# Kernel tuning notes

Measured on AMD Instinct MI355X. Metric: run time of the kernel, lower is better.

The kernel has to match this reference:

```python
import jax, jax.numpy as jnp
import numpy as np

N = 500_000      # total nodes across all graphs in batch
B = 128          # batch_size (number of graphs)
S = 128          # state_size
D = 128          # aggregated_size


def setup_inputs() -> dict:
    key = jax.random.key(0)
    k1, k2, k3, k4, k5, k6 = jax.random.split(key, 6)
    nodes = jax.random.normal(k1, (N, S), dtype=jnp.float32)
    owner_masks = jax.random.randint(k2, (B, N), 0, 2, dtype=jnp.int32)
    # Linear params (torch Linear: y = x @ W.T + b); store W as [in, out] for x @ W
    scale = 1.0 / np.sqrt(S)
    Wt = jax.random.uniform(k3, (S, D), jnp.float32, -scale, scale)
    bt = jax.random.uniform(k4, (D,), jnp.float32, -scale, scale)
    Wg = jax.random.uniform(k5, (S, D), jnp.float32, -scale, scale)
    bg = jax.random.uniform(k6, (D,), jnp.float32, -scale, scale)
    return {"nodes": nodes, "owner_masks": owner_masks,
            "Wt": Wt, "bt": bt, "Wg": Wg, "bg": bg}


def reference(nodes, owner_masks, Wt, bt, Wg, bg):
    # gates = sigmoid(nodes @ Wg + bg)   [N, D]
    gates = jax.nn.sigmoid(nodes @ Wg + bg)
    # data = nodes @ Wt + bt             [N, D]
    data = nodes @ Wt + bt
    # pooled = owner_masks.float() @ (data * gates)   [B, D]
    return owner_masks.astype(jnp.float32) @ (data * gates)
```

## Files before the change

### kernel.cpp

```cpp
#include <hip/hip_runtime.h>


#define NTOT   500000
#define NBLK   500
#define NCHUNK 15625

typedef unsigned long long u64;
typedef unsigned int u32;

typedef __attribute__((ext_vector_type(8))) unsigned short ushort8;
typedef __bf16 bf16x8 __attribute__((ext_vector_type(8)));
typedef __attribute__((ext_vector_type(4))) float f32x4;

static __device__ __forceinline__ unsigned short f2bf(float f) {
  u32 u = __float_as_uint(f);
  u += 0x7fffu + ((u >> 16) & 1u);
  return (unsigned short)(u >> 16);
}

static __device__ __forceinline__ u64 pack4(unsigned short a, unsigned short b,
                                            unsigned short c, unsigned short d) {
  return (u64)a | ((u64)b << 16) | ((u64)c << 32) | ((u64)d << 48);
}

static __device__ __forceinline__ u32 bits2bf2(u32 byte, int j) {
  return ((byte >> j) & 1u ? 0x3F80u : 0u) | ((byte >> (j + 1)) & 1u ? 0x3F800000u : 0u);
}

template <bool ATOMIC>
__global__ __launch_bounds__(256, 2)
void agg_main(const float* __restrict__ nodes, const int* __restrict__ masks,
              const float* __restrict__ Wt, const float* __restrict__ bt,
              const float* __restrict__ Wg, const float* __restrict__ bg,
              float* __restrict__ outp) {
  __shared__ __align__(16) unsigned short nodes_s[32][136];
  __shared__ __align__(16) u64 bits[128][17];
  __shared__ __align__(16) unsigned short vt_s[128][40];

  const int tid = threadIdx.x;
  const int lane = tid & 63;
  const int w = tid >> 6;
  const int q = lane >> 4;
  const int r = lane & 15;

  const int bid = blockIdx.x;
  const int c0 = (int)(((long long)bid * NCHUNK) / NBLK);
  const int c1 = (int)(((long long)(bid + 1) * NCHUNK) / NBLK);
  const int nch = c1 - c0;
  const int n0 = c0 * 32;

  bf16x8 Wf[2][4][2];
  float btr[2], bgr[2];
#pragma unroll
  for (int nt = 0; nt < 2; ++nt) {
    const int d = w * 32 + nt * 16 + r;
    btr[nt] = bt[d];
    bgr[nt] = bg[d];
#pragma unroll
    for (int ks = 0; ks < 4; ++ks) {
      ushort8 ft, fg;
#pragma unroll
      for (int j = 0; j < 8; ++j) {
        const int k = ks * 32 + q * 8 + j;
        ft[j] = f2bf(Wt[k * 128 + d]);
        fg[j] = f2bf(Wg[k * 128 + d]);
      }
      Wf[0][ks][nt] = __builtin_bit_cast(bf16x8, ft);
      Wf[1][ks][nt] = __builtin_bit_cast(bf16x8, fg);
    }
  }

  {
    const int row0 = w * 32;
    int cur[32], nxt[32];
#pragma unroll
    for (int k = 0; k < 32; ++k)
      cur[k] = masks[(size_t)(row0 + k) * NTOT + n0 + lane];
#pragma unroll
    for (int g = 0; g < 16; ++g) {
      if (g < 15) {
#pragma unroll
        for (int k = 0; k < 32; ++k)
          nxt[k] = masks[(size_t)(row0 + k) * NTOT + n0 + (g + 1) * 64 + lane];
      }
      u64 v = 0;
#pragma unroll
      for (int k = 0; k < 32; ++k) {
        u64 bl = __ballot(cur[k] != 0);
        if (lane == k) v = bl;
      }
      if (lane < 32) bits[row0 + lane][g] = v;
      if (g < 15) {
#pragma unroll
        for (int k = 0; k < 32; ++k) cur[k] = nxt[k];
      }
    }
  }

  f32x4 acc[8][2];
  const f32x4 fzero = {0.f, 0.f, 0.f, 0.f};
#pragma unroll
  for (int i = 0; i < 8; ++i) {
    acc[i][0] = fzero;
    acc[i][1] = fzero;
  }

  float4 nf[4];
  auto issue = [&](int cloc) {
    const int k0 = n0 + cloc * 32;
#pragma unroll
    for (int it = 0; it < 4; ++it) {
      const int flat = it * 256 + tid;
      const int nrow = flat >> 5, nc4 = flat & 31;
      nf[it] = *(const float4*)(nodes + (size_t)(k0 + nrow) * 128 + nc4 * 4);
    }
  };

  issue(0);
  __syncthreads();

  const u32* bitw = (const u32*)bits;

  for (int c = 0; c < nch; ++c) {
    if (c) __syncthreads();
#pragma unroll
    for (int it = 0; it < 4; ++it) {
      const int flat = it * 256 + tid;
      const int nrow = flat >> 5, nc4 = flat & 31;
      *(u64*)&nodes_s[nrow][nc4 * 4] =
          pack4(f2bf(nf[it].x), f2bf(nf[it].y), f2bf(nf[it].z), f2bf(nf[it].w));
    }
    __syncthreads();
    if (c + 1 < nch) issue(c + 1);

    f32x4 aD[2][2], aG[2][2];
#pragma unroll
    for (int i = 0; i < 2; ++i)
#pragma unroll
      for (int j = 0; j < 2; ++j) { aD[i][j] = fzero; aG[i][j] = fzero; }
#pragma unroll
    for (int ks = 0; ks < 4; ++ks) {
      bf16x8 a0 = *(const bf16x8*)&nodes_s[r][ks * 32 + q * 8];
      bf16x8 a1 = *(const bf16x8*)&nodes_s[16 + r][ks * 32 + q * 8];
#pragma unroll
      for (int nt = 0; nt < 2; ++nt) {
        aD[0][nt] = __builtin_amdgcn_mfma_f32_16x16x32_bf16(a0, Wf[0][ks][nt], aD[0][nt], 0, 0, 0);
        aD[1][nt] = __builtin_amdgcn_mfma_f32_16x16x32_bf16(a1, Wf[0][ks][nt], aD[1][nt], 0, 0, 0);
        aG[0][nt] = __builtin_amdgcn_mfma_f32_16x16x32_bf16(a0, Wf[1][ks][nt], aG[0][nt], 0, 0, 0);
        aG[1][nt] = __builtin_amdgcn_mfma_f32_16x16x32_bf16(a1, Wf[1][ks][nt], aG[1][nt], 0, 0, 0);
      }
    }

#pragma unroll
    for (int mt = 0; mt < 2; ++mt)
#pragma unroll
      for (int nt = 0; nt < 2; ++nt) {
        const int d = w * 32 + nt * 16 + r;
        unsigned short t[4];
#pragma unroll
        for (int reg = 0; reg < 4; ++reg) {
          const float x = aD[mt][nt][reg] + btr[nt];
          const float g = aG[mt][nt][reg] + bgr[nt];
          t[reg] = f2bf(x / (1.f + __expf(-g)));
        }
        *(u64*)&vt_s[d][mt * 16 + q * 4] = pack4(t[0], t[1], t[2], t[3]);
      }

    bf16x8 bfr[2];
#pragma unroll
    for (int nt = 0; nt < 2; ++nt)
      bfr[nt] = *(const bf16x8*)&vt_s[w * 32 + nt * 16 + r][q * 8];
#pragma unroll
    for (int mt = 0; mt < 8; ++mt) {
      const u32 dw = bitw[(mt * 16 + r) * 34 + c];
      const u32 byte = (dw >> (q * 8)) & 0xffu;
      u32 p0 = bits2bf2(byte, 0), p1 = bits2bf2(byte, 2);
      u32 p2 = bits2bf2(byte, 4), p3 = bits2bf2(byte, 6);
      u32 af[4] = {p0, p1, p2, p3};
      bf16x8 a = __builtin_bit_cast(bf16x8, *(ushort8*)af);
#pragma unroll
      for (int nt = 0; nt < 2; ++nt)
        acc[mt][nt] = __builtin_amdgcn_mfma_f32_16x16x32_bf16(a, bfr[nt], acc[mt][nt], 0, 0, 0);
    }
  }

#pragma unroll
  for (int mt = 0; mt < 8; ++mt)
#pragma unroll
    for (int nt = 0; nt < 2; ++nt)
#pragma unroll
      for (int reg = 0; reg < 4; ++reg) {
        const int b = mt * 16 + q * 4 + reg;
        const int d = w * 32 + nt * 16 + r;
        if (ATOMIC)
          atomicAdd(&outp[b * 128 + d], acc[mt][nt][reg]);
        else
          outp[(size_t)bid * 16384 + b * 128 + d] = acc[mt][nt][reg];
      }
}

__global__ __launch_bounds__(256)
void agg_reduce(const float* __restrict__ part, float* __restrict__ out) {
  const int gid = blockIdx.x * 256 + threadIdx.x;
  const int i = gid & 16383;
  const int grp = gid >> 14;
  const float* p = part + (size_t)grp * 125 * 16384 + i;
  float s = 0.f;
#pragma unroll 5
  for (int g = 0; g < 125; ++g) s += p[(size_t)g * 16384];
  atomicAdd(&out[i], s);
}

extern "C" void kernel_launch(void* const* d_in, const int* in_sizes, int n_in,
                              void* d_out, int out_size, void* d_ws, size_t ws_size,
                              hipStream_t stream) {
  const float* nodes = (const float*)d_in[0];
  const int*   masks = (const int*)d_in[1];
  const float* Wt    = (const float*)d_in[2];
  const float* bt    = (const float*)d_in[3];
  const float* Wg    = (const float*)d_in[4];
  const float* bg    = (const float*)d_in[5];
  float* out = (float*)d_out;

  hipMemsetAsync(d_out, 0, (size_t)out_size * sizeof(float), stream);

  const size_t need = (size_t)NBLK * 16384 * sizeof(float);
  if (ws_size >= need) {
    agg_main<false><<<NBLK, 256, 0, stream>>>(nodes, masks, Wt, bt, Wg, bg, (float*)d_ws);
    agg_reduce<<<256, 256, 0, stream>>>((const float*)d_ws, out);
  } else {
    agg_main<true><<<NBLK, 256, 0, stream>>>(nodes, masks, Wt, bt, Wg, bg, out);
  }
}
```

Baseline: 562.5 us.

## Use 512-thread blocks, 512 workgroups, and vectorized mask-to-bit packing

Doubles the block size to 8 waves, so each wave owns 16 output columns instead of 32 and each block stages half as many node rows per thread. Mask bitpacking switches from per-element ballots to int4 vector loads, with each lane packing 16 consecutive nodes per row. The grid becomes 512 blocks so the chunk split can use a shift, and the reduce kernel is adjusted to match. The sigmoid division is also replaced with a hardware reciprocal. These changes aim to raise occupancy and memory-level parallelism on the bandwidth-bound mask read, at the cost of more barrier participants and a changed bit layout.

```diff
diff --git a/kernel.cpp b/kernel.cpp
--- a/kernel.cpp
+++ b/kernel.cpp
@@ -2,7 +2,7 @@
 
 
 #define NTOT   500000
-#define NBLK   500
+#define NBLK   512
 #define NCHUNK 15625
 
 typedef unsigned long long u64;
@@ -12,15 +12,14 @@
 typedef __bf16 bf16x8 __attribute__((ext_vector_type(8)));
 typedef __attribute__((ext_vector_type(4))) float f32x4;
 
-static __device__ __forceinline__ unsigned short f2bf(float f) {
+static __device__ __forceinline__ u32 f2bf1(float f) {
   u32 u = __float_as_uint(f);
   u += 0x7fffu + ((u >> 16) & 1u);
-  return (unsigned short)(u >> 16);
-}
-
-static __device__ __forceinline__ u64 pack4(unsigned short a, unsigned short b,
-                                            unsigned short c, unsigned short d) {
-  return (u64)a | ((u64)b << 16) | ((u64)c << 32) | ((u64)d << 48);
+  return u >> 16;
+}
+
+static __device__ __forceinline__ u32 f2bf2(float a, float b) {
+  return f2bf1(a) | (f2bf1(b) << 16);
 }
 
 static __device__ __forceinline__ u32 bits2bf2(u32 byte, int j) {
@@ -28,7 +27,7 @@
 }
 
 template <bool ATOMIC>
-__global__ __launch_bounds__(256, 2)
+__global__ __launch_bounds__(512, 4)
 void agg_main(const float* __restrict__ nodes, const int* __restrict__ masks,
               const float* __restrict__ Wt, const float* __restrict__ bt,
               const float* __restrict__ Wg, const float* __restrict__ bg,
@@ -44,73 +43,66 @@
   const int r = lane & 15;
 
   const int bid = blockIdx.x;
-  const int c0 = (int)(((long long)bid * NCHUNK) / NBLK);
-  const int c1 = (int)(((long long)(bid + 1) * NCHUNK) / NBLK);
+  const int c0 = (int)(((long long)bid * NCHUNK) >> 9);
+  const int c1 = (int)(((long long)(bid + 1) * NCHUNK) >> 9);
   const int nch = c1 - c0;
   const int n0 = c0 * 32;
 
-  bf16x8 Wf[2][4][2];
-  float btr[2], bgr[2];
-#pragma unroll
-  for (int nt = 0; nt < 2; ++nt) {
-    const int d = w * 32 + nt * 16 + r;
-    btr[nt] = bt[d];
-    bgr[nt] = bg[d];
+  {
+    const int row0 = w * 16;
+    int cb = 16 * lane;
+    if (cb >= nch * 32) cb = 0;
+    int4 cur[4], nxt[4];
+    auto ldrow = [&](int rr, int4* dst) {
+      const int* p = masks + (size_t)(row0 + rr) * NTOT + n0 + cb;
+#pragma unroll
+      for (int i = 0; i < 4; ++i) dst[i] = *(const int4*)(p + 4 * i);
+    };
+    ldrow(0, cur);
+#pragma unroll 4
+    for (int rr = 0; rr < 16; ++rr) {
+      if (rr < 15) ldrow(rr + 1, nxt);
+      const int* m = (const int*)cur;
+      u32 b = 0;
+#pragma unroll
+      for (int e = 0; e < 16; ++e) b |= (u32)(m[e] != 0) << e;
+      ((unsigned short*)bits)[(row0 + rr) * 68 + lane] = (unsigned short)b;
+#pragma unroll
+      for (int i = 0; i < 4; ++i) cur[i] = nxt[i];
+    }
+  }
+
+  bf16x8 Wf[2][4];
+  float btr, bgr;
+  {
+    const int d = w * 16 + r;
+    btr = bt[d];
+    bgr = bg[d];
 #pragma unroll
     for (int ks = 0; ks < 4; ++ks) {
-      ushort8 ft, fg;
-#pragma unroll
-      for (int j = 0; j < 8; ++j) {
-        const int k = ks * 32 + q * 8 + j;
-        ft[j] = f2bf(Wt[k * 128 + d]);
-        fg[j] = f2bf(Wg[k * 128 + d]);
+      u32 wv[4], gv[4];
+#pragma unroll
+      for (int j = 0; j < 4; ++j) {
+        const int k = ks * 32 + q * 8 + 2 * j;
+        wv[j] = f2bf2(Wt[k * 128 + d], Wt[(k + 1) * 128 + d]);
+        gv[j] = f2bf2(Wg[k * 128 + d], Wg[(k + 1) * 128 + d]);
       }
-      Wf[0][ks][nt] = __builtin_bit_cast(bf16x8, ft);
-      Wf[1][ks][nt] = __builtin_bit_cast(bf16x8, fg);
-    }
-  }
-
-  {
-    const int row0 = w * 32;
-    int cur[32], nxt[32];
-#pragma unroll
-    for (int k = 0; k < 32; ++k)
-      cur[k] = masks[(size_t)(row0 + k) * NTOT + n0 + lane];
-#pragma unroll
-    for (int g = 0; g < 16; ++g) {
-      if (g < 15) {
-#pragma unroll
-        for (int k = 0; k < 32; ++k)
-          nxt[k] = masks[(size_t)(row0 + k) * NTOT + n0 + (g + 1) * 64 + lane];
-      }
-      u64 v = 0;
-#pragma unroll
-      for (int k = 0; k < 32; ++k) {
-        u64 bl = __ballot(cur[k] != 0);
-        if (lane == k) v = bl;
-      }
-      if (lane < 32) bits[row0 + lane][g] = v;
-      if (g < 15) {
-#pragma unroll
-        for (int k = 0; k < 32; ++k) cur[k] = nxt[k];
-      }
-    }
-  }
-
-  f32x4 acc[8][2];
+      Wf[0][ks] = __builtin_bit_cast(bf16x8, *(ushort8*)wv);
+      Wf[1][ks] = __builtin_bit_cast(bf16x8, *(ushort8*)gv);
+    }
+  }
+
   const f32x4 fzero = {0.f, 0.f, 0.f, 0.f};
-#pragma unroll
-  for (int i = 0; i < 8; ++i) {
-    acc[i][0] = fzero;
-    acc[i][1] = fzero;
-  }
-
-  float4 nf[4];
+  f32x4 acc[8];
+#pragma unroll
+  for (int i = 0; i < 8; ++i) acc[i] = fzero;
+
+  float4 nf[2];
   auto issue = [&](int cloc) {
     const int k0 = n0 + cloc * 32;
 #pragma unroll
-    for (int it = 0; it < 4; ++it) {
-      const int flat = it * 256 + tid;
+    for (int it = 0; it < 2; ++it) {
+      const int flat = it * 512 + tid;
       const int nrow = flat >> 5, nc4 = flat & 31;
       nf[it] = *(const float4*)(nodes + (size_t)(k0 + nrow) * 128 + nc4 * 4);
     }
@@ -124,79 +116,69 @@
   for (int c = 0; c < nch; ++c) {
     if (c) __syncthreads();
 #pragma unroll
-    for (int it = 0; it < 4; ++it) {
-      const int flat = it * 256 + tid;
+    for (int it = 0; it < 2; ++it) {
+      const int flat = it * 512 + tid;
       const int nrow = flat >> 5, nc4 = flat & 31;
-      *(u64*)&nodes_s[nrow][nc4 * 4] =
-          pack4(f2bf(nf[it].x), f2bf(nf[it].y), f2bf(nf[it].z), f2bf(nf[it].w));
+      const u32 lo = f2bf2(nf[it].x, nf[it].y);
+      const u32 hi = f2bf2(nf[it].z, nf[it].w);
+      *(u64*)&nodes_s[nrow][nc4 * 4] = (u64)lo | ((u64)hi << 32);
     }
     __syncthreads();
     if (c + 1 < nch) issue(c + 1);
 
-    f32x4 aD[2][2], aG[2][2];
-#pragma unroll
-    for (int i = 0; i < 2; ++i)
-#pragma unroll
-      for (int j = 0; j < 2; ++j) { aD[i][j] = fzero; aG[i][j] = fzero; }
+    f32x4 aD[2], aG[2];
+    aD[0] = fzero; aD[1] = fzero; aG[0] = fzero; aG[1] = fzero;
 #pragma unroll
     for (int ks = 0; ks < 4; ++ks) {
       bf16x8 a0 = *(const bf16x8*)&nodes_s[r][ks * 32 + q * 8];
       bf16x8 a1 = *(const bf16x8*)&nodes_s[16 + r][ks * 32 + q * 8];
-#pragma unroll
-      for (int nt = 0; nt < 2; ++nt) {
-        aD[0][nt] = __builtin_amdgcn_mfma_f32_16x16x32_bf16(a0, Wf[0][ks][nt], aD[0][nt], 0, 0, 0);
-        aD[1][nt] = __builtin_amdgcn_mfma_f32_16x16x32_bf16(a1, Wf[0][ks][nt], aD[1][nt], 0, 0, 0);
-        aG[0][nt] = __builtin_amdgcn_mfma_f32_16x16x32_bf16(a0, Wf[1][ks][nt], aG[0][nt], 0, 0, 0);
-        aG[1][nt] = __builtin_amdgcn_mfma_f32_16x16x32_bf16(a1, Wf[1][ks][nt], aG[1][nt], 0, 0, 0);
+      aD[0] = __builtin_amdgcn_mfma_f32_16x16x32_bf16(a0, Wf[0][ks], aD[0], 0, 0, 0);
+      aD[1] = __builtin_amdgcn_mfma_f32_16x16x32_bf16(a1, Wf[0][ks], aD[1], 0, 0, 0);
+      aG[0] = __builtin_amdgcn_mfma_f32_16x16x32_bf16(a0, Wf[1][ks], aG[0], 0, 0, 0);
+      aG[1] = __builtin_amdgcn_mfma_f32_16x16x32_bf16(a1, Wf[1][ks], aG[1], 0, 0, 0);
+    }
+
+    const int d = w * 16 + r;
+#pragma unroll
+    for (int mt = 0; mt < 2; ++mt) {
+      float v[4];
+#pragma unroll
+      for (int reg = 0; reg < 4; ++reg) {
+        const float x = aD[mt][reg] + btr;
+        const float g = aG[mt][reg] + bgr;
+        v[reg] = x * __builtin_amdgcn_rcpf(1.f + __expf(-g));
       }
-    }
-
-#pragma unroll
-    for (int mt = 0; mt < 2; ++mt)
-#pragma unroll
-      for (int nt = 0; nt < 2; ++nt) {
-        const int d = w * 32 + nt * 16 + r;
-        unsigned short t[4];
-#pragma unroll
-        for (int reg = 0; reg < 4; ++reg) {
-          const float x = aD[mt][nt][reg] + btr[nt];
-          const float g = aG[mt][nt][reg] + bgr[nt];
-          t[reg] = f2bf(x / (1.f + __expf(-g)));
-        }
-        *(u64*)&vt_s[d][mt * 16 + q * 4] = pack4(t[0], t[1], t[2], t[3]);
-      }
-
-    bf16x8 bfr[2];
-#pragma unroll
-    for (int nt = 0; nt < 2; ++nt)
-      bfr[nt] = *(const bf16x8*)&vt_s[w * 32 + nt * 16 + r][q * 8];
+      const u32 lo = f2bf2(v[0], v[1]);
+      const u32 hi = f2bf2(v[2], v[3]);
+      *(u64*)&vt_s[d][mt * 16 + q * 4] = (u64)lo | ((u64)hi << 32);
+    }
+
+    bf16x8 bfr = *(const bf16x8*)&vt_s[d][q * 8];
 #pragma unroll
     for (int mt = 0; mt < 8; ++mt) {
       const u32 dw = bitw[(mt * 16 + r) * 34 + c];
       const u32 byte = (dw >> (q * 8)) & 0xffu;
-      u32 p0 = bits2bf2(byte, 0), p1 = bits2bf2(byte, 2);
-      u32 p2 = bits2bf2(byte, 4), p3 = bits2bf2(byte, 6);
-      u32 af[4] = {p0, p1, p2, p3};
-      bf16x8 a = __builtin_bit_cast(bf16x8, *(ushort8*)af);
-#pragma unroll
-      for (int nt = 0; nt < 2; ++nt)
-        acc[mt][nt] = __builtin_amdgcn_mfma_f32_16x16x32_bf16(a, bfr[nt], acc[mt][nt], 0, 0, 0);
+      u32 p[4];
+      p[0] = bits2bf2(byte, 0);
+      p[1] = bits2bf2(byte, 2);
+      p[2] = bits2bf2(byte, 4);
+      p[3] = bits2bf2(byte, 6);
+      bf16x8 a = __builtin_bit_cast(bf16x8, *(ushort8*)p);
+      acc[mt] = __builtin_amdgcn_mfma_f32_16x16x32_bf16(a, bfr, acc[mt], 0, 0, 0);
     }
   }
 
 #pragma unroll
   for (int mt = 0; mt < 8; ++mt)
 #pragma unroll
-    for (int nt = 0; nt < 2; ++nt)
-#pragma unroll
-      for (int reg = 0; reg < 4; ++reg) {
-        const int b = mt * 16 + q * 4 + reg;
-        const int d = w * 32 + nt * 16 + r;
-        if (ATOMIC)
-          atomicAdd(&outp[b * 128 + d], acc[mt][nt][reg]);
-        else
-          outp[(size_t)bid * 16384 + b * 128 + d] = acc[mt][nt][reg];
-      }
+    for (int reg = 0; reg < 4; ++reg) {
+      const int b = mt * 16 + q * 4 + reg;
+      const int d = w * 16 + r;
+      if (ATOMIC)
+        atomicAdd(&outp[b * 128 + d], acc[mt][reg]);
+      else
+        outp[(size_t)bid * 16384 + b * 128 + d] = acc[mt][reg];
+    }
 }
 
 __global__ __launch_bounds__(256)
@@ -204,10 +186,10 @@
   const int gid = blockIdx.x * 256 + threadIdx.x;
   const int i = gid & 16383;
   const int grp = gid >> 14;
-  const float* p = part + (size_t)grp * 125 * 16384 + i;
+  const float* p = part + (size_t)grp * 64 * 16384 + i;
   float s = 0.f;
-#pragma unroll 5
-  for (int g = 0; g < 125; ++g) s += p[(size_t)g * 16384];
+#pragma unroll 8
+  for (int g = 0; g < 64; ++g) s += p[(size_t)g * 16384];
   atomicAdd(&out[i], s);
 }
 
@@ -222,13 +204,13 @@
   const float* bg    = (const float*)d_in[5];
   float* out = (float*)d_out;
 
-  hipMemsetAsync(d_out, 0, (size_t)out_size * sizeof(float), stream);
+  (void)hipMemsetAsync(d_out, 0, (size_t)out_size * sizeof(float), stream);
 
   const size_t need = (size_t)NBLK * 16384 * sizeof(float);
   if (ws_size >= need) {
-    agg_main<false><<<NBLK, 256, 0, stream>>>(nodes, masks, Wt, bt, Wg, bg, (float*)d_ws);
-    agg_reduce<<<256, 256, 0, stream>>>((const float*)d_ws, out);
+    agg_main<false><<<NBLK, 512, 0, stream>>>(nodes, masks, Wt, bt, Wg, bg, (float*)d_ws);
+    agg_reduce<<<512, 256, 0, stream>>>((const float*)d_ws, out);
   } else {
-    agg_main<true><<<NBLK, 256, 0, stream>>>(nodes, masks, Wt, bt, Wg, bg, out);
-  }
-}
+    agg_main<true><<<NBLK, 512, 0, stream>>>(nodes, masks, Wt, bt, Wg, bg, out);
+  }
+}
```

Result: faster. 535.6 us (-4.8%).
